# Kernel optimization log

Hardware: AMD Instinct MI355X
Metric: run time of the kernel (lower is better)

## Reference

```python
import jax, jax.numpy as jnp
import numpy as np

# Lattice / network constants (from init_kwargs surrogate for the quimb fPEPS)
Lx, Ly, D, CHI, PHYS = 6, 6, 4, 16, 2
H = 64                      # nn_hidden_dim
ETA = 1e-3                  # nn_eta
NSITES = Lx * Ly
NB = (Ly - 1) * (Lx - 1)    # compressed vertical bonds per column boundary grid
PROJ_LEN = NB * 2 * (CHI * D) * CHI  # P (chi*D x chi) and Q (chi x chi*D) per bond
BATCH = 1024


def setup_inputs() -> dict:
    key = jax.random.key(0)
    ks = jax.random.split(key, 6)
    x = jax.random.randint(ks[0], (BATCH, NSITES), 0, 2)
    # dense surrogate of the packed symmetry-block PEPS params: (l, r, u, d, phys)
    peps = jax.random.normal(ks[1], (Lx, Ly, D, D, D, D, PHYS), dtype=jnp.float32) * 0.3
    # base projector parameter vector (in the original these come from dynamic
    # insert_proj_peps packing; here they are the packed baseline the MLP corrects)
    base_proj = jax.random.normal(ks[2], (PROJ_LEN,), dtype=jnp.float32) * 0.15
    W1 = jax.random.normal(ks[3], (NSITES, H), dtype=jnp.float32) / np.sqrt(NSITES)
    b1 = jnp.zeros((H,), dtype=jnp.float32)
    W2 = jax.random.normal(ks[4], (H, PROJ_LEN), dtype=jnp.float32) / np.sqrt(H)
    b2 = jnp.zeros((PROJ_LEN,), dtype=jnp.float32)
    return {"x": x, "peps": peps, "base_proj": base_proj,
            "W1": W1, "b1": b1, "W2": W2, "b2": b2}


def _site(peps, xi, r, c):
    # select physical index (occupation) then clip boundary bonds to dim 1
    A = peps[r, c, :, :, :, :, xi[r * Ly + c]]  # (l, rt, u, d)
    if c == 0:
        A = A[0:1]
    if c == Ly - 1:
        A = A[:, 0:1]
    if r == 0:
        A = A[:, :, 0:1]
    if r == Lx - 1:
        A = A[:, :, :, 0:1]
    return A


def _amplitude(xi, peps, base_proj, W1, b1, W2, b2):
    # MLP correction to projector params (proj_params_vec += eta * mlp(x_i))
    h = jnp.maximum(xi.astype(jnp.float32) @ W1 + b1, 0.0)
    vec = base_proj + ETA * (h @ W2 + b2)
    pq = vec.reshape(Ly - 1, Lx - 1, 2, CHI * D * CHI)
    Pm = pq[:, :, 0].reshape(Ly - 1, Lx - 1, CHI * D, CHI)
    Qm = pq[:, :, 1].reshape(Ly - 1, Lx - 1, CHI, CHI * D)
    # boundary MPS from column 0; interior vertical bonds zero-padded D -> CHI
    Ms = []
    for r in range(Lx):
        A = _site(peps, xi, r, 0)[0]        # (rt, u, d)
        A = jnp.transpose(A, (1, 2, 0))     # (u, d, rt)
        pu = CHI - A.shape[0] if A.shape[0] > 1 else 0
        pd = CHI - A.shape[1] if A.shape[1] > 1 else 0
        Ms.append(jnp.pad(A, ((0, pu), (0, pd), (0, 0))))
    # sweep columns left -> right, absorbing then compressing via projectors
    for c in range(1, Ly):
        grown = []
        for r in range(Lx):
            A = _site(peps, xi, r, c)       # (l, rt, a, b)
            T = jnp.einsum('udl,lrab->uadbr', Ms[r], A)
            s = T.shape
            grown.append(T.reshape(s[0] * s[1], s[2] * s[3], s[4]))
        comp = []
        for r in range(Lx):
            M = grown[r]
            if r < Lx - 1:  # down bond compression: (chi*D) -> chi
                M = jnp.einsum('udr,dc->ucr', M, Pm[c - 1, r])
            if r > 0:       # up bond compression: (chi*D) -> chi
                M = jnp.einsum('udr,cu->cdr', M, Qm[c - 1, r - 1])
            comp.append(M)
        Ms = comp
    # final boundary MPS has right-dim 1; contract the chain to a scalar
    v = Ms[0][0, :, 0]
    for r in range(1, Lx):
        v = v @ Ms[r][:, :, 0]
    return v[0]


def reference(x, peps, base_proj, W1, b1, W2, b2):
    return jax.vmap(lambda xi: _amplitude(xi, peps, base_proj, W1, b1, W2, b2))(x)
```

## Files before the change

### kernel.cpp

```cpp
#include <hip/hip_runtime.h>


constexpr int   kNSites = 36;
constexpr int   kProj   = 51200;
constexpr float kEta    = 0.001f;

__device__ __forceinline__ float4 f4fma(float s, float4 a, float4 c) {
    c.x = fmaf(s, a.x, c.x); c.y = fmaf(s, a.y, c.y);
    c.z = fmaf(s, a.z, c.z); c.w = fmaf(s, a.w, c.w);
    return c;
}
__device__ __forceinline__ unsigned short f2bf(float f) {
    union { float f; unsigned int u; } v; v.f = f;
    unsigned int r = v.u + 0x7FFFu + ((v.u >> 16) & 1u);
    return (unsigned short)(r >> 16);
}
__device__ __forceinline__ float bf2f(unsigned int h) {
    union { unsigned int u; float f; } v; v.u = h << 16;
    return v.f;
}
__device__ __forceinline__ void cvt4(const uint2 q, const float4 b, float* dst) {
    float4 o;
    o.x = b.x + kEta * bf2f(q.x & 0xffffu);
    o.y = b.y + kEta * bf2f(q.x >> 16);
    o.z = b.z + kEta * bf2f(q.y & 0xffffu);
    o.w = b.w + kEta * bf2f(q.y >> 16);
    *reinterpret_cast<float4*>(dst) = o;
}

__global__ __launch_bounds__(256)
void h_prep(const int* __restrict__ x,
            const float* __restrict__ W1,
            const float* __restrict__ b1,
            float* __restrict__ hf,
            int batch)
{
    const int tid = threadIdx.x;
    const int s   = blockIdx.x * 4 + (tid >> 6);
    const int k   = tid & 63;
    if (s >= batch) return;
    float a = b1[k];
    for (int j = 0; j < kNSites; ++j)
        a = fmaf((float)x[s * kNSites + j], W1[j * 64 + k], a);
    hf[s * 64 + k] = fmaxf(a, 0.0f);
}

__global__ __launch_bounds__(256)
void gen_q(const float* __restrict__ hf,
           const float* __restrict__ W2,
           const float* __restrict__ b2,
           unsigned short* __restrict__ qout,
           int s0, int send)
{
    __shared__ float hT[64 * 68];
    const int tid   = threadIdx.x;
    const int sbase = s0 + blockIdx.x * 64;
    const int ns    = blockIdx.y;

#pragma unroll
    for (int ii = 0; ii < 4; ++ii) {
        int sl = (tid >> 4) + 16 * ii;
        int sA = sbase + sl; if (sA >= send) sA = send - 1;
        float4 hv = *reinterpret_cast<const float4*>(hf + sA * 64 + (tid & 15) * 4);
        int kb = (tid & 15) * 4;
        hT[(kb + 0) * 68 + sl] = hv.x;
        hT[(kb + 1) * 68 + sl] = hv.y;
        hT[(kb + 2) * 68 + sl] = hv.z;
        hT[(kb + 3) * 68 + sl] = hv.w;
    }
    __syncthreads();

    const int sgrp = tid >> 6;
    const int col  = ns * 256 + (tid & 63) * 4;
    float4 acc[16];
#pragma unroll
    for (int i = 0; i < 16; ++i) acc[i] = make_float4(0, 0, 0, 0);
    const float* wp = W2 + col;
#pragma unroll 8
    for (int k = 0; k < 64; ++k) {
        float4 w = *reinterpret_cast<const float4*>(wp + (size_t)k * kProj);
#pragma unroll
        for (int s4 = 0; s4 < 4; ++s4) {
            float4 hv = *reinterpret_cast<const float4*>(&hT[k * 68 + sgrp * 16 + s4 * 4]);
            acc[s4 * 4 + 0] = f4fma(hv.x, w, acc[s4 * 4 + 0]);
            acc[s4 * 4 + 1] = f4fma(hv.y, w, acc[s4 * 4 + 1]);
            acc[s4 * 4 + 2] = f4fma(hv.z, w, acc[s4 * 4 + 2]);
            acc[s4 * 4 + 3] = f4fma(hv.w, w, acc[s4 * 4 + 3]);
        }
    }
    float4 bb = *reinterpret_cast<const float4*>(b2 + col);
#pragma unroll
    for (int i = 0; i < 16; ++i) {
        int sA = sbase + sgrp * 16 + i;
        if (sA < send) {
            ushort4 uv;
            uv.x = f2bf(acc[i].x + bb.x); uv.y = f2bf(acc[i].y + bb.y);
            uv.z = f2bf(acc[i].z + bb.z); uv.w = f2bf(acc[i].w + bb.w);
            *reinterpret_cast<ushort4*>(qout + (size_t)(sA - s0) * kProj + col) = uv;
        }
    }
}

constexpr int OFF_MS   = 0;
constexpr int OFF_MS0  = 4096;
constexpr int OFF_MS5  = 4160;
constexpr int OFF_P    = 4224;
constexpr int OFF_Q    = 5248;
constexpr int OFF_MOLD = 6336;
constexpr int OFF_M2H  = 10432;
constexpr int OFF_A2   = 12480;
constexpr int OFF_VB   = 12736;
constexpr int LTOT     = 12752;

__global__ __launch_bounds__(256, 2)
void tn_con(const int* __restrict__ x,
            const float* __restrict__ peps,
            const float* __restrict__ base_proj,
            const unsigned short* __restrict__ qc,
            float* __restrict__ out,
            int s0, int send)
{
    __shared__ __align__(16) float L[LTOT];
    __shared__ int xl[kNSites];

    const int tid  = threadIdx.x;
    const int wid  = tid >> 6;
    const int lane = tid & 63;
    const int sIdx = s0 + blockIdx.x;
    int sAbs = sIdx; if (sAbs >= send) sAbs = send - 1;

    if (tid < kNSites) xl[tid] = x[sAbs * kNSites + tid];
    for (int i = tid; i < 4224; i += 256) L[i] = 0.0f;
    __syncthreads();

    for (int idx = tid; idx < 512; idx += 256) {
        int rr = idx >> 6, u = (idx >> 4) & 3, d = (idx >> 2) & 3, l = idx & 3;
        if (rr >= 6) continue;
        int p = xl[rr * 6];
        if (rr == 0) {
            if (u == 0) L[OFF_MS0 + d * 4 + l] = peps[l * 32 + d * 2 + p];
        } else if (rr == 5) {
            if (d == 0) L[OFF_MS5 + u * 4 + l] = peps[5 * 3072 + l * 32 + u * 8 + p];
        } else {
            L[OFF_MS + (rr - 1) * 1024 + d * 64 + ((u * 4 + l) ^ ((d & 7) << 2))] =
                peps[rr * 3072 + l * 32 + u * 8 + d * 2 + p];
        }
    }

    const unsigned short* qcs = qc + (size_t)(sAbs - s0) * kProj;
    const int k4 = tid * 4;

    {
        uint2 pq = *reinterpret_cast<const uint2*>(qcs + k4);
        float4 pb = *reinterpret_cast<const float4*>(base_proj + k4);
        cvt4(pq, pb, &L[OFF_P + k4]);
        int lb = tid >> 4, arb = tid & 15;
        int l = lb >> 2, b = lb & 3, a = arb >> 2, rb = arb & 3;
        float v = 0.0f;
        if (a < 1) {
            int p = xl[0 * 6 + 1];
            v = peps[1 * 512 + l * 128 + rb * 32 + a * 8 + b * 2 + p];
        }
        L[OFF_A2 + tid] = v;
    }
    __syncthreads();

    for (int s = 0; s < 30; ++s) {
        const int r = s % 6;

        const int s1 = s + 1;
        const bool hasNext = (s1 < 30);
        const int r1 = s1 % 6, c1 = 1 + s1 / 6;
        const bool doP = hasNext && (r1 <= 4);
        const bool doQ = hasNext && (r1 >= 1);
        uint2 pq = make_uint2(0, 0), qq = pq;
        float4 pb = make_float4(0, 0, 0, 0), qb = pb;
        float a2v = 0.0f;
        if (doP) {
            const int go = ((c1 - 1) * 5 + r1) * 2048 + k4;
            pq = *reinterpret_cast<const uint2*>(qcs + go);
            pb = *reinterpret_cast<const float4*>(base_proj + go);
        }
        if (doQ) {
            const int go = ((c1 - 1) * 5 + (r1 - 1)) * 2048 + 1024 + k4;
            qq = *reinterpret_cast<const uint2*>(qcs + go);
            qb = *reinterpret_cast<const float4*>(base_proj + go);
        }
        if (hasNext) {
            const int adim = (r1 == 0) ? 1 : 4;
            const int bdim = (r1 == 5) ? 1 : 4;
            const int rdim = (c1 == 5) ? 1 : 4;
            int lb = tid >> 4, arb = tid & 15;
            int l = lb >> 2, b = lb & 3, a = arb >> 2, rb = arb & 3;
            if (a < adim && b < bdim && rb < rdim) {
                int p = xl[r1 * 6 + c1];
                a2v = peps[r1 * 3072 + c1 * 512 + l * 128 + rb * 32 + a * 8 + b * 2 + p];
            }
        }

        if (r == 0) {
            if (wid == 0) {
                const int cc = lane >> 2, rb = lane & 3;
                float mold0[16];
#pragma unroll
                for (int i = 0; i < 16; ++i) mold0[i] = 0.0f;
#pragma unroll
                for (int d = 0; d < 16; ++d) {
                    float4 ms = *reinterpret_cast<float4*>(&L[OFF_MS0 + d * 4]);
                    float msl[4] = {ms.x, ms.y, ms.z, ms.w};
#pragma unroll
                    for (int b = 0; b < 4; ++b) {
                        float pv = L[OFF_P + (d * 4 + b) * 16 + cc];
#pragma unroll
                        for (int l = 0; l < 4; ++l)
                            mold0[l * 4 + b] = fmaf(msl[l], pv, mold0[l * 4 + b]);
                    }
                }
                float o = 0.0f;
#pragma unroll
                for (int lb = 0; lb < 16; ++lb)
                    o = fmaf(mold0[lb], L[OFF_A2 + lb * 16 + rb], o);
                L[OFF_MS0 + cc * 4 + rb] = o;
            }
            __syncthreads();
        } else if (r < 5) {
            const int msr = OFF_MS + (r - 1) * 1024;
            {
                const int u = tid >> 4, lb = tid & 15;
                const int l = lb >> 2, b = lb & 3;
                const int pxr = (u & 3) << 2;
                float4 a0 = make_float4(0, 0, 0, 0), a1 = a0, a2 = a0, a3 = a0;
#pragma unroll
                for (int d = 0; d < 16; ++d) {
                    float ms = L[msr + d * 64 + ((u * 4 + l) ^ ((d & 7) << 2))];
                    const int pb2 = OFF_P + (d * 4 + b) * 16;
                    float4 p0 = *reinterpret_cast<float4*>(&L[pb2 + 0]);
                    float4 p1 = *reinterpret_cast<float4*>(&L[pb2 + 4]);
                    float4 p2 = *reinterpret_cast<float4*>(&L[pb2 + 8]);
                    float4 p3 = *reinterpret_cast<float4*>(&L[pb2 + 12]);
                    a0 = f4fma(ms, p0, a0); a1 = f4fma(ms, p1, a1);
                    a2 = f4fma(ms, p2, a2); a3 = f4fma(ms, p3, a3);
                }
                const int mrow = OFF_MOLD + (u * 16 + lb) * 16;
                *reinterpret_cast<float4*>(&L[mrow + (0  ^ pxr)]) = a0;
                *reinterpret_cast<float4*>(&L[mrow + (4  ^ pxr)]) = a1;
                *reinterpret_cast<float4*>(&L[mrow + (8  ^ pxr)]) = a2;
                *reinterpret_cast<float4*>(&L[mrow + (12 ^ pxr)]) = a3;
            }
            __syncthreads();
#pragma unroll
            for (int h = 0; h < 2; ++h) {
                {
                    const int ua = tid >> 2, colq = tid & 3;
                    const int u2 = ua >> 2, a2i = ua & 3;
                    const int pxr = (u2 & 3) << 2;
                    const int cc0 = h * 8 + colq * 2;
                    float4 acc0 = make_float4(0, 0, 0, 0), acc1 = acc0;
#pragma unroll
                    for (int lb = 0; lb < 16; ++lb) {
                        float2 mo = *reinterpret_cast<float2*>(
                            &L[OFF_MOLD + (u2 * 16 + lb) * 16 + (cc0 ^ pxr)]);
                        float4 av = *reinterpret_cast<float4*>(
                            &L[OFF_A2 + lb * 16 + a2i * 4]);
                        acc0 = f4fma(mo.x, av, acc0);
                        acc1 = f4fma(mo.y, av, acc1);
                    }
                    const int m2x = (ua & 7) << 2;
                    *reinterpret_cast<float4*>(
                        &L[OFF_M2H + ua * 32 + (((colq * 2 + 0) * 4) ^ m2x)]) = acc0;
                    *reinterpret_cast<float4*>(
                        &L[OFF_M2H + ua * 32 + (((colq * 2 + 1) * 4) ^ m2x)]) = acc1;
                }
                __syncthreads();
                {
                    const int cq = tid >> 4, cp = tid & 15;
                    const int qb2 = OFF_Q + cq * 68;
                    float ox = 0.0f, oy = 0.0f;
#pragma unroll
                    for (int ua0 = 0; ua0 < 64; ua0 += 4) {
                        float4 q = *reinterpret_cast<float4*>(&L[qb2 + ua0]);
                        float2 m0 = *reinterpret_cast<float2*>(
                            &L[OFF_M2H + (ua0 + 0) * 32 + ((cp * 2) ^ (((ua0 + 0) & 7) << 2))]);
                        float2 m1 = *reinterpret_cast<float2*>(
                            &L[OFF_M2H + (ua0 + 1) * 32 + ((cp * 2) ^ (((ua0 + 1) & 7) << 2))]);
                        float2 m2 = *reinterpret_cast<float2*>(
                            &L[OFF_M2H + (ua0 + 2) * 32 + ((cp * 2) ^ (((ua0 + 2) & 7) << 2))]);
                        float2 m3 = *reinterpret_cast<float2*>(
                            &L[OFF_M2H + (ua0 + 3) * 32 + ((cp * 2) ^ (((ua0 + 3) & 7) << 2))]);
                        ox = fmaf(q.x, m0.x, ox); oy = fmaf(q.x, m0.y, oy);
                        ox = fmaf(q.y, m1.x, ox); oy = fmaf(q.y, m1.y, oy);
                        ox = fmaf(q.z, m2.x, ox); oy = fmaf(q.z, m2.y, oy);
                        ox = fmaf(q.w, m3.x, ox); oy = fmaf(q.w, m3.y, oy);
                    }
                    const int dn = h * 8 + (cp >> 1);
                    const int rb0 = (cp & 1) * 2;
                    float2 o2; o2.x = ox; o2.y = oy;
                    *reinterpret_cast<float2*>(
                        &L[msr + dn * 64 + ((cq * 4 + rb0) ^ ((dn & 7) << 2))]) = o2;
                }
                __syncthreads();
            }
        } else {
            if (wid == 0) {
                {
                    const int u5 = lane >> 2, a5 = lane & 3;
                    float4 ms5 = *reinterpret_cast<float4*>(&L[OFF_MS5 + u5 * 4]);
                    float4 o = make_float4(0, 0, 0, 0);
                    o = f4fma(ms5.x, *reinterpret_cast<float4*>(&L[OFF_A2 + 0 * 16 + a5 * 4]), o);
                    o = f4fma(ms5.y, *reinterpret_cast<float4*>(&L[OFF_A2 + 4 * 16 + a5 * 4]), o);
                    o = f4fma(ms5.z, *reinterpret_cast<float4*>(&L[OFF_A2 + 8 * 16 + a5 * 4]), o);
                    o = f4fma(ms5.w, *reinterpret_cast<float4*>(&L[OFF_A2 + 12 * 16 + a5 * 4]), o);
                    *reinterpret_cast<float4*>(&L[OFF_M2H + lane * 4]) = o;
                }
                {
                    const int cq = lane >> 2, rb = lane & 3;
                    const int qb2 = OFF_Q + cq * 68;
                    float o = 0.0f;
#pragma unroll
                    for (int ua0 = 0; ua0 < 64; ua0 += 4) {
                        float4 q = *reinterpret_cast<float4*>(&L[qb2 + ua0]);
                        o = fmaf(q.x, L[OFF_M2H + (ua0 + 0) * 4 + rb], o);
                        o = fmaf(q.y, L[OFF_M2H + (ua0 + 1) * 4 + rb], o);
                        o = fmaf(q.z, L[OFF_M2H + (ua0 + 2) * 4 + rb], o);
                        o = fmaf(q.w, L[OFF_M2H + (ua0 + 3) * 4 + rb], o);
                    }
                    L[OFF_MS5 + cq * 4 + rb] = o;
                }
            }
            __syncthreads();
        }

        if (doP) cvt4(pq, pb, &L[OFF_P + k4]);
        if (doQ) cvt4(qq, qb, &L[OFF_Q + (k4 >> 6) * 68 + (k4 & 63)]);
        if (hasNext) L[OFF_A2 + tid] = a2v;
        __syncthreads();
    }

    if (wid == 0) {
        if (lane < 16) L[OFF_VB + lane] = L[OFF_MS0 + lane * 4];
        for (int rr = 1; rr < 5; ++rr) {
            float a = 0.0f;
            if (lane < 16) {
#pragma unroll
                for (int u = 0; u < 16; ++u)
                    a = fmaf(L[OFF_VB + u],
                             L[OFF_MS + (rr - 1) * 1024 + lane * 64 +
                               ((u * 4) ^ ((lane & 7) << 2))], a);
            }
            if (lane < 16) L[OFF_VB + lane] = a;
        }
        if (lane == 0 && sIdx < send) {
            float a = 0.0f;
#pragma unroll
            for (int u = 0; u < 16; ++u)
                a = fmaf(L[OFF_VB + u], L[OFF_MS5 + u * 4], a);
            out[sIdx] = a;
        }
    }
}

extern "C" void kernel_launch(void* const* d_in, const int* in_sizes, int n_in,
                              void* d_out, int out_size, void* d_ws, size_t ws_size,
                              hipStream_t stream) {
    const int*   x         = (const int*)d_in[0];
    const float* peps      = (const float*)d_in[1];
    const float* base_proj = (const float*)d_in[2];
    const float* W1        = (const float*)d_in[3];
    const float* b1        = (const float*)d_in[4];
    const float* W2        = (const float*)d_in[5];
    const float* b2        = (const float*)d_in[6];
    float*       out       = (float*)d_out;

    const int batch = in_sizes[0] / kNSites;
    float*          hf = (float*)d_ws;
    unsigned short* q  = (unsigned short*)((char*)d_ws + 262144);

    hipLaunchKernelGGL(h_prep, dim3((batch + 3) / 4), dim3(256), 0, stream,
                       x, W1, b1, hf, batch);

    const size_t perS = (size_t)kProj * 2;
    size_t qbytes = (ws_size > 262144) ? ws_size - 262144 : 0;
    int cs = (int)(qbytes / perS);
    if (cs > batch) cs = batch;
    cs &= ~3;
    if (cs < 4) cs = 4;

    for (int s0 = 0; s0 < batch; s0 += cs) {
        int send = s0 + cs; if (send > batch) send = batch;
        int n = send - s0;
        dim3 g1((n + 63) / 64, 200);
        hipLaunchKernelGGL(gen_q, g1, dim3(256), 0, stream,
                           hf, W2, b2, q, s0, send);
        hipLaunchKernelGGL(tn_con, dim3(n), dim3(256), 0, stream,
                           x, peps, base_proj, q, out, s0, send);
    }
}
```

Measured before the change: 346.7 us.

## Merge two Q-contraction halves into one pass using dead MOLD scratch

The interior-row compression loop used to run two halves, each doing an A2 contraction into M2H and then a Q contraction, with a barrier after every stage. Now both A2 contraction halves run back to back. The second half writes into a no-longer-needed region of the MOLD buffer through a new swizzled address helper (mdead). A single Q contraction pass then has each thread compute two output rows across all 32 columns. This cuts the per-row barriers from four to three and reuses the M-operand loads across two Q rows. The cost is per-lane address selection and possible new LDS bank conflicts in the remapped layout.

```diff
diff --git a/kernel.cpp b/kernel.cpp
--- a/kernel.cpp
+++ b/kernel.cpp
@@ -112,6 +112,13 @@
 constexpr int OFF_VB   = 12736;
 constexpr int LTOT     = 12752;
 
+__device__ __forceinline__ int mdead(int ua, int c3) {
+    int q    = c3 >> 3;
+    int mrow = (ua * 4 + q) ^ ((ua >> 1) & 1);
+    int db   = ((mrow >> 4) & 2) ? 8 : 0;
+    return OFF_MOLD + mrow * 16 + db + ((c3 & 7) ^ ((ua & 1) << 2));
+}
+
 __global__ __launch_bounds__(256, 2)
 void tn_con(const int* __restrict__ x,
             const float* __restrict__ peps,
@@ -248,58 +255,87 @@
                 *reinterpret_cast<float4*>(&L[mrow + (12 ^ pxr)]) = a3;
             }
             __syncthreads();
-#pragma unroll
-            for (int h = 0; h < 2; ++h) {
-                {
-                    const int ua = tid >> 2, colq = tid & 3;
-                    const int u2 = ua >> 2, a2i = ua & 3;
-                    const int pxr = (u2 & 3) << 2;
-                    const int cc0 = h * 8 + colq * 2;
-                    float4 acc0 = make_float4(0, 0, 0, 0), acc1 = acc0;
-#pragma unroll
-                    for (int lb = 0; lb < 16; ++lb) {
-                        float2 mo = *reinterpret_cast<float2*>(
-                            &L[OFF_MOLD + (u2 * 16 + lb) * 16 + (cc0 ^ pxr)]);
-                        float4 av = *reinterpret_cast<float4*>(
-                            &L[OFF_A2 + lb * 16 + a2i * 4]);
-                        acc0 = f4fma(mo.x, av, acc0);
-                        acc1 = f4fma(mo.y, av, acc1);
-                    }
-                    const int m2x = (ua & 7) << 2;
-                    *reinterpret_cast<float4*>(
-                        &L[OFF_M2H + ua * 32 + (((colq * 2 + 0) * 4) ^ m2x)]) = acc0;
-                    *reinterpret_cast<float4*>(
-                        &L[OFF_M2H + ua * 32 + (((colq * 2 + 1) * 4) ^ m2x)]) = acc1;
-                }
-                __syncthreads();
-                {
-                    const int cq = tid >> 4, cp = tid & 15;
-                    const int qb2 = OFF_Q + cq * 68;
-                    float ox = 0.0f, oy = 0.0f;
-#pragma unroll
-                    for (int ua0 = 0; ua0 < 64; ua0 += 4) {
-                        float4 q = *reinterpret_cast<float4*>(&L[qb2 + ua0]);
-                        float2 m0 = *reinterpret_cast<float2*>(
-                            &L[OFF_M2H + (ua0 + 0) * 32 + ((cp * 2) ^ (((ua0 + 0) & 7) << 2))]);
-                        float2 m1 = *reinterpret_cast<float2*>(
-                            &L[OFF_M2H + (ua0 + 1) * 32 + ((cp * 2) ^ (((ua0 + 1) & 7) << 2))]);
-                        float2 m2 = *reinterpret_cast<float2*>(
-                            &L[OFF_M2H + (ua0 + 2) * 32 + ((cp * 2) ^ (((ua0 + 2) & 7) << 2))]);
-                        float2 m3 = *reinterpret_cast<float2*>(
-                            &L[OFF_M2H + (ua0 + 3) * 32 + ((cp * 2) ^ (((ua0 + 3) & 7) << 2))]);
-                        ox = fmaf(q.x, m0.x, ox); oy = fmaf(q.x, m0.y, oy);
-                        ox = fmaf(q.y, m1.x, ox); oy = fmaf(q.y, m1.y, oy);
-                        ox = fmaf(q.z, m2.x, ox); oy = fmaf(q.z, m2.y, oy);
-                        ox = fmaf(q.w, m3.x, ox); oy = fmaf(q.w, m3.y, oy);
-                    }
-                    const int dn = h * 8 + (cp >> 1);
-                    const int rb0 = (cp & 1) * 2;
-                    float2 o2; o2.x = ox; o2.y = oy;
-                    *reinterpret_cast<float2*>(
-                        &L[msr + dn * 64 + ((cq * 4 + rb0) ^ ((dn & 7) << 2))]) = o2;
-                }
-                __syncthreads();
-            }
+            {
+                const int ua = tid >> 2, colq = tid & 3;
+                const int u2 = ua >> 2, a2i = ua & 3;
+                const int pxr = (u2 & 3) << 2;
+                const int cc0 = colq * 2;
+                float4 acc0 = make_float4(0, 0, 0, 0), acc1 = acc0;
+#pragma unroll
+                for (int lb = 0; lb < 16; ++lb) {
+                    float2 mo = *reinterpret_cast<float2*>(
+                        &L[OFF_MOLD + (u2 * 16 + lb) * 16 + (cc0 ^ pxr)]);
+                    float4 av = *reinterpret_cast<float4*>(&L[OFF_A2 + lb * 16 + a2i * 4]);
+                    acc0 = f4fma(mo.x, av, acc0);
+                    acc1 = f4fma(mo.y, av, acc1);
+                }
+                const int m2x = (ua & 7) << 2;
+                *reinterpret_cast<float4*>(
+                    &L[OFF_M2H + ua * 32 + (((colq * 2 + 0) * 4) ^ m2x)]) = acc0;
+                *reinterpret_cast<float4*>(
+                    &L[OFF_M2H + ua * 32 + (((colq * 2 + 1) * 4) ^ m2x)]) = acc1;
+            }
+            __syncthreads();
+            {
+                const int ua = tid >> 2, colq = tid & 3;
+                const int u2 = ua >> 2, a2i = ua & 3;
+                const int pxr = (u2 & 3) << 2;
+                const int cc0 = 8 + colq * 2;
+                float4 acc0 = make_float4(0, 0, 0, 0), acc1 = acc0;
+#pragma unroll
+                for (int lb = 0; lb < 16; ++lb) {
+                    float2 mo = *reinterpret_cast<float2*>(
+                        &L[OFF_MOLD + (u2 * 16 + lb) * 16 + (cc0 ^ pxr)]);
+                    float4 av = *reinterpret_cast<float4*>(&L[OFF_A2 + lb * 16 + a2i * 4]);
+                    acc0 = f4fma(mo.x, av, acc0);
+                    acc1 = f4fma(mo.y, av, acc1);
+                }
+                *reinterpret_cast<float4*>(&L[mdead(ua, (colq * 2 + 0) * 4)]) = acc0;
+                *reinterpret_cast<float4*>(&L[mdead(ua, (colq * 2 + 1) * 4)]) = acc1;
+            }
+            __syncthreads();
+            {
+                const int cp  = tid & 31;
+                const int cq0 = (tid >> 5) * 2;
+                const int qb0 = OFF_Q + cq0 * 68;
+                const int qb1 = OFF_Q + (cq0 + 1) * 68;
+                float ox0 = 0.0f, oy0 = 0.0f, ox1 = 0.0f, oy1 = 0.0f;
+#pragma unroll
+                for (int ua0 = 0; ua0 < 64; ua0 += 4) {
+                    float4 q0 = *reinterpret_cast<float4*>(&L[qb0 + ua0]);
+                    float4 q1 = *reinterpret_cast<float4*>(&L[qb1 + ua0]);
+                    int a0 = (cp < 16) ? (OFF_M2H + (ua0 + 0) * 32 + ((cp * 2) ^ (((ua0 + 0) & 7) << 2)))
+                                       : mdead(ua0 + 0, cp * 2 - 32);
+                    int a1 = (cp < 16) ? (OFF_M2H + (ua0 + 1) * 32 + ((cp * 2) ^ (((ua0 + 1) & 7) << 2)))
+                                       : mdead(ua0 + 1, cp * 2 - 32);
+                    int a2 = (cp < 16) ? (OFF_M2H + (ua0 + 2) * 32 + ((cp * 2) ^ (((ua0 + 2) & 7) << 2)))
+                                       : mdead(ua0 + 2, cp * 2 - 32);
+                    int a3 = (cp < 16) ? (OFF_M2H + (ua0 + 3) * 32 + ((cp * 2) ^ (((ua0 + 3) & 7) << 2)))
+                                       : mdead(ua0 + 3, cp * 2 - 32);
+                    float2 m0 = *reinterpret_cast<float2*>(&L[a0]);
+                    float2 m1 = *reinterpret_cast<float2*>(&L[a1]);
+                    float2 m2 = *reinterpret_cast<float2*>(&L[a2]);
+                    float2 m3 = *reinterpret_cast<float2*>(&L[a3]);
+                    ox0 = fmaf(q0.x, m0.x, ox0); oy0 = fmaf(q0.x, m0.y, oy0);
+                    ox0 = fmaf(q0.y, m1.x, ox0); oy0 = fmaf(q0.y, m1.y, oy0);
+                    ox0 = fmaf(q0.z, m2.x, ox0); oy0 = fmaf(q0.z, m2.y, oy0);
+                    ox0 = fmaf(q0.w, m3.x, ox0); oy0 = fmaf(q0.w, m3.y, oy0);
+                    ox1 = fmaf(q1.x, m0.x, ox1); oy1 = fmaf(q1.x, m0.y, oy1);
+                    ox1 = fmaf(q1.y, m1.x, ox1); oy1 = fmaf(q1.y, m1.y, oy1);
+                    ox1 = fmaf(q1.z, m2.x, ox1); oy1 = fmaf(q1.z, m2.y, oy1);
+                    ox1 = fmaf(q1.w, m3.x, ox1); oy1 = fmaf(q1.w, m3.y, oy1);
+                }
+                const int dn  = cp >> 1;
+                const int rb0 = (cp & 1) * 2;
+                const int wsd = (dn & 7) << 2;
+                float2 o0; o0.x = ox0; o0.y = oy0;
+                float2 o1; o1.x = ox1; o1.y = oy1;
+                *reinterpret_cast<float2*>(
+                    &L[msr + dn * 64 + ((cq0 * 4 + rb0) ^ wsd)]) = o0;
+                *reinterpret_cast<float2*>(
+                    &L[msr + dn * 64 + (((cq0 + 1) * 4 + rb0) ^ wsd)]) = o1;
+            }
+            __syncthreads();
         } else {
             if (wid == 0) {
                 {
```

Result: no change. 341.5 us (-1.5%).

## Restructure interior-row contraction into full-width M2 buffer with register-blocked threads

Applied to the files above, without the earlier changes.

Interior rows no longer split the second and third contractions into two column halves. The full intermediate M2 goes into a larger shared buffer, which removes two barriers per row per column. Each thread now computes a 2x2 register block in all three stages, reusing loaded P, A2 and Q values across two outputs to cut LDS traffic. Shared memory use grows by about 8 KB per block, which may affect how many blocks fit per CU at launch bounds of 2.

```diff
diff --git a/kernel.cpp b/kernel.cpp
--- a/kernel.cpp
+++ b/kernel.cpp
@@ -107,10 +107,10 @@
 constexpr int OFF_P    = 4224;
 constexpr int OFF_Q    = 5248;
 constexpr int OFF_MOLD = 6336;
-constexpr int OFF_M2H  = 10432;
-constexpr int OFF_A2   = 12480;
-constexpr int OFF_VB   = 12736;
-constexpr int LTOT     = 12752;
+constexpr int OFF_M2   = 10432;
+constexpr int OFF_A2   = 14528;
+constexpr int OFF_VB   = 14784;
+constexpr int LTOT     = 14800;
 
 __global__ __launch_bounds__(256, 2)
 void tn_con(const int* __restrict__ x,
@@ -226,80 +226,98 @@
         } else if (r < 5) {
             const int msr = OFF_MS + (r - 1) * 1024;
             {
-                const int u = tid >> 4, lb = tid & 15;
+                const int up = tid >> 5;
+                const int lb = (tid >> 1) & 15;
+                const int chalf = tid & 1;
                 const int l = lb >> 2, b = lb & 3;
-                const int pxr = (u & 3) << 2;
-                float4 a0 = make_float4(0, 0, 0, 0), a1 = a0, a2 = a0, a3 = a0;
+                const int cbase = chalf * 8;
+                float4 m00 = make_float4(0,0,0,0), m01 = m00, m10 = m00, m11 = m00;
 #pragma unroll
                 for (int d = 0; d < 16; ++d) {
-                    float ms = L[msr + d * 64 + ((u * 4 + l) ^ ((d & 7) << 2))];
-                    const int pb2 = OFF_P + (d * 4 + b) * 16;
-                    float4 p0 = *reinterpret_cast<float4*>(&L[pb2 + 0]);
-                    float4 p1 = *reinterpret_cast<float4*>(&L[pb2 + 4]);
-                    float4 p2 = *reinterpret_cast<float4*>(&L[pb2 + 8]);
-                    float4 p3 = *reinterpret_cast<float4*>(&L[pb2 + 12]);
-                    a0 = f4fma(ms, p0, a0); a1 = f4fma(ms, p1, a1);
-                    a2 = f4fma(ms, p2, a2); a3 = f4fma(ms, p3, a3);
-                }
-                const int mrow = OFF_MOLD + (u * 16 + lb) * 16;
-                *reinterpret_cast<float4*>(&L[mrow + (0  ^ pxr)]) = a0;
-                *reinterpret_cast<float4*>(&L[mrow + (4  ^ pxr)]) = a1;
-                *reinterpret_cast<float4*>(&L[mrow + (8  ^ pxr)]) = a2;
-                *reinterpret_cast<float4*>(&L[mrow + (12 ^ pxr)]) = a3;
+                    const int swd = (d & 7) << 2;
+                    float ms0 = L[msr + d * 64 + ((up * 4 + l) ^ swd)];
+                    float ms1 = L[msr + d * 64 + (((up + 8) * 4 + l) ^ swd)];
+                    const int pbase = OFF_P + (d * 4 + b) * 16 + cbase;
+                    float4 p0 = *reinterpret_cast<float4*>(&L[pbase + 0]);
+                    float4 p1 = *reinterpret_cast<float4*>(&L[pbase + 4]);
+                    m00 = f4fma(ms0, p0, m00); m01 = f4fma(ms0, p1, m01);
+                    m10 = f4fma(ms1, p0, m10); m11 = f4fma(ms1, p1, m11);
+                }
+                const int sw0 = (up & 3) << 2;
+                const int r0w = OFF_MOLD + (up * 16 + lb) * 16;
+                const int r1w = OFF_MOLD + ((up + 8) * 16 + lb) * 16;
+                *reinterpret_cast<float4*>(&L[r0w + ((cbase + 0) ^ sw0)]) = m00;
+                *reinterpret_cast<float4*>(&L[r0w + ((cbase + 4) ^ sw0)]) = m01;
+                *reinterpret_cast<float4*>(&L[r1w + ((cbase + 0) ^ sw0)]) = m10;
+                *reinterpret_cast<float4*>(&L[r1w + ((cbase + 4) ^ sw0)]) = m11;
             }
             __syncthreads();
-#pragma unroll
-            for (int h = 0; h < 2; ++h) {
-                {
-                    const int ua = tid >> 2, colq = tid & 3;
-                    const int u2 = ua >> 2, a2i = ua & 3;
-                    const int pxr = (u2 & 3) << 2;
-                    const int cc0 = h * 8 + colq * 2;
-                    float4 acc0 = make_float4(0, 0, 0, 0), acc1 = acc0;
-#pragma unroll
-                    for (int lb = 0; lb < 16; ++lb) {
-                        float2 mo = *reinterpret_cast<float2*>(
-                            &L[OFF_MOLD + (u2 * 16 + lb) * 16 + (cc0 ^ pxr)]);
-                        float4 av = *reinterpret_cast<float4*>(
-                            &L[OFF_A2 + lb * 16 + a2i * 4]);
-                        acc0 = f4fma(mo.x, av, acc0);
-                        acc1 = f4fma(mo.y, av, acc1);
-                    }
-                    const int m2x = (ua & 7) << 2;
-                    *reinterpret_cast<float4*>(
-                        &L[OFF_M2H + ua * 32 + (((colq * 2 + 0) * 4) ^ m2x)]) = acc0;
-                    *reinterpret_cast<float4*>(
-                        &L[OFF_M2H + ua * 32 + (((colq * 2 + 1) * 4) ^ m2x)]) = acc1;
-                }
-                __syncthreads();
-                {
-                    const int cq = tid >> 4, cp = tid & 15;
-                    const int qb2 = OFF_Q + cq * 68;
-                    float ox = 0.0f, oy = 0.0f;
-#pragma unroll
-                    for (int ua0 = 0; ua0 < 64; ua0 += 4) {
-                        float4 q = *reinterpret_cast<float4*>(&L[qb2 + ua0]);
-                        float2 m0 = *reinterpret_cast<float2*>(
-                            &L[OFF_M2H + (ua0 + 0) * 32 + ((cp * 2) ^ (((ua0 + 0) & 7) << 2))]);
-                        float2 m1 = *reinterpret_cast<float2*>(
-                            &L[OFF_M2H + (ua0 + 1) * 32 + ((cp * 2) ^ (((ua0 + 1) & 7) << 2))]);
-                        float2 m2 = *reinterpret_cast<float2*>(
-                            &L[OFF_M2H + (ua0 + 2) * 32 + ((cp * 2) ^ (((ua0 + 2) & 7) << 2))]);
-                        float2 m3 = *reinterpret_cast<float2*>(
-                            &L[OFF_M2H + (ua0 + 3) * 32 + ((cp * 2) ^ (((ua0 + 3) & 7) << 2))]);
-                        ox = fmaf(q.x, m0.x, ox); oy = fmaf(q.x, m0.y, oy);
-                        ox = fmaf(q.y, m1.x, ox); oy = fmaf(q.y, m1.y, oy);
-                        ox = fmaf(q.z, m2.x, ox); oy = fmaf(q.z, m2.y, oy);
-                        ox = fmaf(q.w, m3.x, ox); oy = fmaf(q.w, m3.y, oy);
-                    }
-                    const int dn = h * 8 + (cp >> 1);
-                    const int rb0 = (cp & 1) * 2;
-                    float2 o2; o2.x = ox; o2.y = oy;
-                    *reinterpret_cast<float2*>(
-                        &L[msr + dn * 64 + ((cq * 4 + rb0) ^ ((dn & 7) << 2))]) = o2;
-                }
-                __syncthreads();
-            }
+            {
+                const int uap = tid >> 3;
+                const int ccp = tid & 7;
+                const int u2 = uap >> 2, a = uap & 3;
+                const int sw2 = (u2 & 3) << 2;
+                const int cc0 = ccp * 2;
+                float4 a00 = make_float4(0,0,0,0), a01 = a00, a10 = a00, a11 = a00;
+#pragma unroll
+                for (int lb = 0; lb < 16; ++lb) {
+                    float2 mo0 = *reinterpret_cast<float2*>(
+                        &L[OFF_MOLD + (u2 * 16 + lb) * 16 + (cc0 ^ sw2)]);
+                    float2 mo1 = *reinterpret_cast<float2*>(
+                        &L[OFF_MOLD + ((u2 + 8) * 16 + lb) * 16 + (cc0 ^ sw2)]);
+                    float4 av = *reinterpret_cast<float4*>(&L[OFF_A2 + lb * 16 + a * 4]);
+                    a00 = f4fma(mo0.x, av, a00); a01 = f4fma(mo0.y, av, a01);
+                    a10 = f4fma(mo1.x, av, a10); a11 = f4fma(mo1.y, av, a11);
+                }
+                const int swm = (uap & 7) << 2;
+                *reinterpret_cast<float4*>(
+                    &L[OFF_M2 + uap * 64 + (((cc0    ) * 4) ^ swm)]) = a00;
+                *reinterpret_cast<float4*>(
+                    &L[OFF_M2 + uap * 64 + (((cc0 + 1) * 4) ^ swm)]) = a01;
+                *reinterpret_cast<float4*>(
+                    &L[OFF_M2 + (uap + 32) * 64 + (((cc0    ) * 4) ^ swm)]) = a10;
+                *reinterpret_cast<float4*>(
+                    &L[OFF_M2 + (uap + 32) * 64 + (((cc0 + 1) * 4) ^ swm)]) = a11;
+            }
+            __syncthreads();
+            {
+                const int cq0 = (tid >> 5) * 2;
+                const int cp  = tid & 31;
+                const int qb0 = OFF_Q + cq0 * 68;
+                const int qb1 = qb0 + 68;
+                float ox0 = 0.0f, oy0 = 0.0f, ox1 = 0.0f, oy1 = 0.0f;
+#pragma unroll
+                for (int ua0 = 0; ua0 < 64; ua0 += 4) {
+                    float4 q0 = *reinterpret_cast<float4*>(&L[qb0 + ua0]);
+                    float4 q1 = *reinterpret_cast<float4*>(&L[qb1 + ua0]);
+                    float2 m0 = *reinterpret_cast<float2*>(
+                        &L[OFF_M2 + (ua0 + 0) * 64 + ((cp * 2) ^ (((ua0 + 0) & 7) << 2))]);
+                    float2 m1 = *reinterpret_cast<float2*>(
+                        &L[OFF_M2 + (ua0 + 1) * 64 + ((cp * 2) ^ (((ua0 + 1) & 7) << 2))]);
+                    float2 m2 = *reinterpret_cast<float2*>(
+                        &L[OFF_M2 + (ua0 + 2) * 64 + ((cp * 2) ^ (((ua0 + 2) & 7) << 2))]);
+                    float2 m3 = *reinterpret_cast<float2*>(
+                        &L[OFF_M2 + (ua0 + 3) * 64 + ((cp * 2) ^ (((ua0 + 3) & 7) << 2))]);
+                    ox0 = fmaf(q0.x, m0.x, ox0); oy0 = fmaf(q0.x, m0.y, oy0);
+                    ox0 = fmaf(q0.y, m1.x, ox0); oy0 = fmaf(q0.y, m1.y, oy0);
+                    ox0 = fmaf(q0.z, m2.x, ox0); oy0 = fmaf(q0.z, m2.y, oy0);
+                    ox0 = fmaf(q0.w, m3.x, ox0); oy0 = fmaf(q0.w, m3.y, oy0);
+                    ox1 = fmaf(q1.x, m0.x, ox1); oy1 = fmaf(q1.x, m0.y, oy1);
+                    ox1 = fmaf(q1.y, m1.x, ox1); oy1 = fmaf(q1.y, m1.y, oy1);
+                    ox1 = fmaf(q1.z, m2.x, ox1); oy1 = fmaf(q1.z, m2.y, oy1);
+                    ox1 = fmaf(q1.w, m3.x, ox1); oy1 = fmaf(q1.w, m3.y, oy1);
+                }
+                const int dn  = cp >> 1;
+                const int rb0 = (cp & 1) * 2;
+                const int wsd = (dn & 7) << 2;
+                float2 o0; o0.x = ox0; o0.y = oy0;
+                float2 o1; o1.x = ox1; o1.y = oy1;
+                *reinterpret_cast<float2*>(
+                    &L[msr + dn * 64 + ((cq0 * 4 + rb0) ^ wsd)]) = o0;
+                *reinterpret_cast<float2*>(
+                    &L[msr + dn * 64 + (((cq0 + 1) * 4 + rb0) ^ wsd)]) = o1;
+            }
+            __syncthreads();
         } else {
             if (wid == 0) {
                 {
@@ -310,7 +328,7 @@
                     o = f4fma(ms5.y, *reinterpret_cast<float4*>(&L[OFF_A2 + 4 * 16 + a5 * 4]), o);
                     o = f4fma(ms5.z, *reinterpret_cast<float4*>(&L[OFF_A2 + 8 * 16 + a5 * 4]), o);
                     o = f4fma(ms5.w, *reinterpret_cast<float4*>(&L[OFF_A2 + 12 * 16 + a5 * 4]), o);
-                    *reinterpret_cast<float4*>(&L[OFF_M2H + lane * 4]) = o;
+                    *reinterpret_cast<float4*>(&L[OFF_M2 + lane * 4]) = o;
                 }
                 {
                     const int cq = lane >> 2, rb = lane & 3;
@@ -319,10 +337,10 @@
 #pragma unroll
                     for (int ua0 = 0; ua0 < 64; ua0 += 4) {
                         float4 q = *reinterpret_cast<float4*>(&L[qb2 + ua0]);
-                        o = fmaf(q.x, L[OFF_M2H + (ua0 + 0) * 4 + rb], o);
-                        o = fmaf(q.y, L[OFF_M2H + (ua0 + 1) * 4 + rb], o);
-                        o = fmaf(q.z, L[OFF_M2H + (ua0 + 2) * 4 + rb], o);
-                        o = fmaf(q.w, L[OFF_M2H + (ua0 + 3) * 4 + rb], o);
+                        o = fmaf(q.x, L[OFF_M2 + (ua0 + 0) * 4 + rb], o);
+                        o = fmaf(q.y, L[OFF_M2 + (ua0 + 1) * 4 + rb], o);
+                        o = fmaf(q.z, L[OFF_M2 + (ua0 + 2) * 4 + rb], o);
+                        o = fmaf(q.w, L[OFF_M2 + (ua0 + 3) * 4 + rb], o);
                     }
                     L[OFF_MS5 + cq * 4 + rb] = o;
                 }
```

Measured after the change: 292.1 us. 1.19x faster.
